# Kernel optimization log

Measured on AMD Instinct MI355X. Metric: run time of the kernel, lower is better.

The kernel has to match this reference:

```python
import jax, jax.numpy as jnp
import numpy as np

B, L, D, K = 1024, 50, 128, 20
NI, NL, NT = 100000, 10000, 2000  # items, locs, times


def _emb(k, n, d):
    e = jax.random.normal(k, (n, d), dtype=jnp.float32) * 0.02
    return e.at[0].set(0.0)  # padding_idx=0


def setup_inputs() -> dict:
    key = jax.random.key(0)
    ks = jax.random.split(key, 40)
    inp = {}
    inp['item'] = jax.random.randint(ks[0], (B, L), 0, NI)
    inp['locs'] = jax.random.randint(ks[1], (B,), 0, NL)
    inp['times'] = jax.random.randint(ks[2], (B,), 0, NT)
    inp['session_emb'] = jax.random.normal(ks[3], (B, 1, D), dtype=jnp.float32)
    # embedding tables
    inp['loc_emb'] = _emb(ks[4], NL, D)
    inp['time_emb'] = _emb(ks[5], NT, D)
    inp['item_emb'] = _emb(ks[6], NI, D)
    # sampled fixed-fanout neighbor tables Hg[edge]['neighbor']
    inp['nb_IL'] = jax.random.randint(ks[7], (NL, K), 0, NI)   # item neighbors of locs
    inp['nb_TL'] = jax.random.randint(ks[8], (NL, K), 0, NT)   # time neighbors of locs
    inp['nb_IT'] = jax.random.randint(ks[9], (NT, K), 0, NI)   # item neighbors of times
    inp['nb_LT'] = jax.random.randint(ks[10], (NT, K), 0, NL)  # loc neighbors of times
    inp['nb_II'] = jax.random.randint(ks[11], (NI, K), 0, NI)  # item neighbors of items
    inp['nb_LI'] = jax.random.randint(ks[12], (NI, K), 0, NL)  # loc neighbors of items
    inp['nb_TI'] = jax.random.randint(ks[13], (NI, K), 0, NT)  # time neighbors of items
    # 7 HeteAggregator params: Linear(2D -> D) + ReLU
    s = 1.0 / np.sqrt(2 * D)
    names = ['IL', 'TL', 'IT', 'LT', 'II', 'LI', 'TI']
    for i, nm in enumerate(names):
        inp['W_' + nm] = jax.random.uniform(ks[14 + i], (2 * D, D), jnp.float32, -s, s)
        inp['b_' + nm] = jnp.zeros((D,), jnp.float32)
    # 3 SemanticAttention params: Linear(D->D,bias)+tanh, Linear(D->1,no bias)
    s2 = 1.0 / np.sqrt(D)
    for i, nm in enumerate(['l', 't', 'i']):
        inp['Ws_' + nm] = jax.random.uniform(ks[24 + 3 * i], (D, D), jnp.float32, -s2, s2)
        inp['bs_' + nm] = jnp.zeros((D,), jnp.float32)
        inp['q_' + nm] = jax.random.uniform(ks[25 + 3 * i], (D, 1), jnp.float32, -s2, s2)
    return inp


def hete_agg(h_self, h_neigh, W, b):
    # h_self: [N, D]; h_neigh: [N, K, D] -> mean-aggregate, concat, linear, relu
    agg = h_neigh.mean(axis=1)
    return jax.nn.relu(jnp.concatenate([h_self, agg], axis=-1) @ W + b)


def sem_att(z, Ws, bs, q):
    # HAN-style semantic attention. z: [N, M, D]
    w = jnp.tanh(z @ Ws + bs) @ q          # [N, M, 1]
    beta = jax.nn.softmax(w.mean(axis=0), axis=0)  # [M, 1]
    return (beta[None] * z).sum(axis=1)    # [N, D]


def reference(item, locs, times, session_emb,
              loc_emb, time_emb, item_emb,
              nb_IL, nb_TL, nb_IT, nb_LT, nb_II, nb_LI, nb_TI,
              W_IL, b_IL, W_TL, b_TL, W_IT, b_IT, W_LT, b_LT,
              W_II, b_II, W_LI, b_LI, W_TI, b_TI,
              Ws_l, bs_l, q_l, Ws_t, bs_t, q_t, Ws_i, bs_i, q_i):
    iids = item.reshape(-1)  # [B*L]
    h_l_IL = hete_agg(loc_emb[locs], item_emb[nb_IL[locs]], W_IL, b_IL)
    h_l_TL = hete_agg(loc_emb[locs], time_emb[nb_TL[locs]], W_TL, b_TL)
    h_t_IT = hete_agg(time_emb[times], item_emb[nb_IT[times]], W_IT, b_IT)
    h_t_LT = hete_agg(time_emb[times], loc_emb[nb_LT[times]], W_LT, b_LT)
    h_i_II = hete_agg(item_emb[iids], item_emb[nb_II[iids]], W_II, b_II)
    h_i_LI = hete_agg(item_emb[iids], loc_emb[nb_LI[iids]], W_LI, b_LI)
    h_i_TI = hete_agg(item_emb[iids], time_emb[nb_TI[iids]], W_TI, b_TI)
    h_s = session_emb.squeeze(1)  # [B, D]
    h_l_stack = jnp.stack([h_l_IL, h_l_TL, h_s], axis=1)
    h_t_stack = jnp.stack([h_t_IT, h_t_LT, h_s], axis=1)
    h_i_stack = jnp.stack([h_i_II, h_i_TI, h_i_LI], axis=1)
    h_items = sem_att(h_i_stack, Ws_i, bs_i, q_i)
    h_locs = sem_att(h_l_stack, Ws_l, bs_l, q_l)
    h_times = sem_att(h_t_stack, Ws_t, bs_t, q_t)
    return (h_items, h_locs, h_times)
```

## Files before the change

### kernel.cpp

```cpp
#include <hip/hip_runtime.h>
#include <hip/hip_fp16.h>

#define DD 128
#define KK 20
#define TRR 16

typedef unsigned int uint_t;
typedef unsigned short ushort_t;
typedef unsigned char uchar_t;
typedef _Float16 f16x8 __attribute__((ext_vector_type(8)));
typedef _Float16 f16x2 __attribute__((ext_vector_type(2)));
typedef float f32x4 __attribute__((ext_vector_type(4)));
typedef float f32x2 __attribute__((ext_vector_type(2)));

union UH { __half h; ushort_t s; };
union UF { f16x2 v[4]; uint4 u4; };

#if __has_builtin(__builtin_amdgcn_cvt_scalef32_pk_f16_fp8)
#define HAVE_SCALEF32 1
#endif

__device__ __forceinline__ float fast_tanh(float x) {
  const float e = __expf(2.f * x);
  return 1.f - 2.f / (e + 1.f);
}

__device__ __forceinline__ void f8acc(f16x2* a, const uint2 v) {
#ifdef HAVE_SCALEF32
  a[0] += __builtin_amdgcn_cvt_scalef32_pk_f16_fp8(v.x, 1.0f, false);
  a[1] += __builtin_amdgcn_cvt_scalef32_pk_f16_fp8(v.x, 1.0f, true);
  a[2] += __builtin_amdgcn_cvt_scalef32_pk_f16_fp8(v.y, 1.0f, false);
  a[3] += __builtin_amdgcn_cvt_scalef32_pk_f16_fp8(v.y, 1.0f, true);
#else
  f32x2 p;
  p = __builtin_amdgcn_cvt_pk_f32_fp8(v.x, false);
  a[0] += __builtin_amdgcn_cvt_pkrtz(p[0], p[1]);
  p = __builtin_amdgcn_cvt_pk_f32_fp8(v.x, true);
  a[1] += __builtin_amdgcn_cvt_pkrtz(p[0], p[1]);
  p = __builtin_amdgcn_cvt_pk_f32_fp8(v.y, false);
  a[2] += __builtin_amdgcn_cvt_pkrtz(p[0], p[1]);
  p = __builtin_amdgcn_cvt_pk_f32_fp8(v.y, true);
  a[3] += __builtin_amdgcn_cvt_pkrtz(p[0], p[1]);
#endif
}

struct CvtArgs {
  const float* item; const float* loc; const float* timet;
  ushort_t* dst16; uchar_t* dst8;
};

__global__ __launch_bounds__(256)
void k_cvt3(CvtArgs a) {
  const int t = blockIdx.x * blockDim.x + threadIdx.x;
  const float* src;
  if (t < 1600000) src = a.item + (size_t)t * 8;
  else if (t < 1760000) src = a.loc + ((size_t)t - 1600000) * 8;
  else src = a.timet + ((size_t)t - 1760000) * 8;
  const float4* ip = reinterpret_cast<const float4*>(src);
  const float4 x = ip[0], y = ip[1];
  UH h[8];
  h[0].h = __float2half_rn(x.x); h[1].h = __float2half_rn(x.y);
  h[2].h = __float2half_rn(x.z); h[3].h = __float2half_rn(x.w);
  h[4].h = __float2half_rn(y.x); h[5].h = __float2half_rn(y.y);
  h[6].h = __float2half_rn(y.z); h[7].h = __float2half_rn(y.w);
  uint4 o;
  o.x = (uint_t)h[0].s | ((uint_t)h[1].s << 16);
  o.y = (uint_t)h[2].s | ((uint_t)h[3].s << 16);
  o.z = (uint_t)h[4].s | ((uint_t)h[5].s << 16);
  o.w = (uint_t)h[6].s | ((uint_t)h[7].s << 16);
  reinterpret_cast<uint4*>(a.dst16)[t] = o;
  uint_t p0 = __builtin_amdgcn_cvt_pk_fp8_f32(x.x, x.y, 0u, false);
  p0 = __builtin_amdgcn_cvt_pk_fp8_f32(x.z, x.w, p0, true);
  uint_t p1 = __builtin_amdgcn_cvt_pk_fp8_f32(y.x, y.y, 0u, false);
  p1 = __builtin_amdgcn_cvt_pk_fp8_f32(y.z, y.w, p1, true);
  uint2 q; q.x = p0; q.y = p1;
  reinterpret_cast<uint2*>(a.dst8)[t] = q;
}

struct PackArgs {
  const float* src[10];
  ushort_t* dst;
};

__global__ __launch_bounds__(256)
void k_pack10(PackArgs a) {
  const int b = blockIdx.x, tid = threadIdx.x;
  int job, tin;
  size_t doff;
  if (b < 112) {
    job = b >> 4; tin = ((b & 15) << 8) | tid;
    doff = (size_t)job * 32768;
  } else {
    job = 7 + ((b - 112) >> 3); tin = (((b - 112) & 7) << 8) | tid;
    doff = 7ull * 32768 + (size_t)(job - 7) * 16384;
  }
  const float* W = a.src[job];
  const int l = tin & 63;
  const int ktnt = tin >> 6;
  const int nt = ktnt & 7;
  const int kt = ktnt >> 3;
  const int col = nt * 16 + (l & 15);
  const int kb = kt * 32 + ((l >> 4) << 3);
  UH h[8];
#pragma unroll
  for (int j = 0; j < 8; ++j) h[j].h = __float2half_rn(W[(size_t)(kb + j) * DD + col]);
  uint4 o;
  o.x = (uint_t)h[0].s | ((uint_t)h[1].s << 16);
  o.y = (uint_t)h[2].s | ((uint_t)h[3].s << 16);
  o.z = (uint_t)h[4].s | ((uint_t)h[5].s << 16);
  o.w = (uint_t)h[6].s | ((uint_t)h[7].s << 16);
  *reinterpret_cast<uint4*>(a.dst + doff + (size_t)ktnt * 512 + l * 8) = o;
}

struct MegaArgs {
  const int* item_idx; const ushort_t* item_t;
  const int* nbI[3]; const uchar_t* embI[3]; const ushort_t* pWI[3]; const float* bI[3];
  const ushort_t* pWsI; const float* bsI; const float* qI;
  ushort_t* hI; float* wsumI;
  const int* sidx[2]; const ushort_t* st[2];
  const int* nbS[2][2]; const uchar_t* embS[2][2];
  const ushort_t* pWS[2][2]; const float* bS[2][2];
  const ushort_t* pWsS[2]; const float* bsS[2]; const float* qS[2];
  const float* session;
  ushort_t* hS[2]; float* wsumS[2];
};

__global__ __launch_bounds__(256, 7)
void k_mega(MegaArgs a) {
  __shared__ int ids[TRR];
  __shared__ int nidx[3][TRR][KK];
  __shared__ __align__(16) ushort_t xs[TRR][4 * DD + 8];
  __shared__ float red[4][TRR];

  const int tid = threadIdx.x;
  const int l = tid & 63;
  const int w = tid >> 6;
  const int bid = blockIdx.x;

  const bool isS = bid < 128;
  const int g = isS ? (bid >> 6) : 0;
  const int bl = isS ? (bid & 63) : (bid - 128);
  const int n0 = bl * TRR;

  const int* sidx;
  const ushort_t* selft;
  const int* nb_[3];
  const uchar_t* emb_[3];
  const ushort_t* pW_[3];
  const float* bias_[3];
  const ushort_t* pws; const float* bss; const float* qp;
  ushort_t* hd; float* wbase;
  if (!isS) {
    sidx = a.item_idx; selft = a.item_t;
    nb_[0] = a.nbI[0]; nb_[1] = a.nbI[1]; nb_[2] = a.nbI[2];
    emb_[0] = a.embI[0]; emb_[1] = a.embI[1]; emb_[2] = a.embI[2];
    pW_[0] = a.pWI[0]; pW_[1] = a.pWI[1]; pW_[2] = a.pWI[2];
    bias_[0] = a.bI[0]; bias_[1] = a.bI[1]; bias_[2] = a.bI[2];
    pws = a.pWsI; bss = a.bsI; qp = a.qI;
    hd = a.hI; wbase = a.wsumI;
  } else if (g == 0) {
    sidx = a.sidx[0]; selft = a.st[0];
    nb_[0] = a.nbS[0][0]; nb_[1] = a.nbS[0][1]; nb_[2] = nullptr;
    emb_[0] = a.embS[0][0]; emb_[1] = a.embS[0][1]; emb_[2] = nullptr;
    pW_[0] = a.pWS[0][0]; pW_[1] = a.pWS[0][1]; pW_[2] = nullptr;
    bias_[0] = a.bS[0][0]; bias_[1] = a.bS[0][1]; bias_[2] = nullptr;
    pws = a.pWsS[0]; bss = a.bsS[0]; qp = a.qS[0];
    hd = a.hS[0]; wbase = a.wsumS[0];
  } else {
    sidx = a.sidx[1]; selft = a.st[1];
    nb_[0] = a.nbS[1][0]; nb_[1] = a.nbS[1][1]; nb_[2] = nullptr;
    emb_[0] = a.embS[1][0]; emb_[1] = a.embS[1][1]; emb_[2] = nullptr;
    pW_[0] = a.pWS[1][0]; pW_[1] = a.pWS[1][1]; pW_[2] = nullptr;
    bias_[0] = a.bS[1][0]; bias_[1] = a.bS[1][1]; bias_[2] = nullptr;
    pws = a.pWsS[1]; bss = a.bsS[1]; qp = a.qS[1];
    hd = a.hS[1]; wbase = a.wsumS[1];
  }

  if (tid < TRR) ids[tid] = sidx[n0 + tid];
  __syncthreads();

  const int gr = tid >> 4;
  const int gsl = tid & 15;

#pragma unroll
  for (int e = 0; e < 3; ++e) {
    if (nb_[e]) {
      for (int t = tid; t < TRR * KK; t += 256) {
        const int rr = t / KK, kk = t - rr * KK;
        nidx[e][rr][kk] = nb_[e][(size_t)ids[rr] * KK + kk];
      }
    }
  }
  *reinterpret_cast<uint4*>(&xs[gr][gsl * 8]) =
      *reinterpret_cast<const uint4*>(selft + ((size_t)ids[gr] << 7) + gsl * 8);
  __syncthreads();

  const _Float16 sch = (_Float16)(1.f / KK);
  const f16x2 scv = (f16x2){sch, sch};
  if (!isS) {
    UF A0, A1, A2;
#pragma unroll
    for (int i = 0; i < 4; ++i) {
      A0.v[i] = (f16x2)0; A1.v[i] = (f16x2)0; A2.v[i] = (f16x2)0;
    }
#pragma unroll
    for (int kb = 0; kb < KK; kb += 4) {
      uint2 u0[4], u1[4], u2[4];
#pragma unroll
      for (int j = 0; j < 4; ++j)
        u0[j] = *reinterpret_cast<const uint2*>(emb_[0] + ((size_t)nidx[0][gr][kb + j] << 7) + gsl * 8);
#pragma unroll
      for (int j = 0; j < 4; ++j)
        u1[j] = *reinterpret_cast<const uint2*>(emb_[1] + ((size_t)nidx[1][gr][kb + j] << 7) + gsl * 8);
#pragma unroll
      for (int j = 0; j < 4; ++j)
        u2[j] = *reinterpret_cast<const uint2*>(emb_[2] + ((size_t)nidx[2][gr][kb + j] << 7) + gsl * 8);
#pragma unroll
      for (int j = 0; j < 4; ++j) {
        f8acc(A0.v, u0[j]); f8acc(A1.v, u1[j]); f8acc(A2.v, u2[j]);
      }
    }
#pragma unroll
    for (int i = 0; i < 4; ++i) {
      A0.v[i] *= scv; A1.v[i] *= scv; A2.v[i] *= scv;
    }
    *reinterpret_cast<uint4*>(&xs[gr][1 * DD + gsl * 8]) = A0.u4;
    *reinterpret_cast<uint4*>(&xs[gr][2 * DD + gsl * 8]) = A1.u4;
    *reinterpret_cast<uint4*>(&xs[gr][3 * DD + gsl * 8]) = A2.u4;
  } else {
    UF A0, A1;
#pragma unroll
    for (int i = 0; i < 4; ++i) { A0.v[i] = (f16x2)0; A1.v[i] = (f16x2)0; }
#pragma unroll
    for (int kb = 0; kb < KK; kb += 5) {
      uint2 u0[5], u1[5];
#pragma unroll
      for (int j = 0; j < 5; ++j)
        u0[j] = *reinterpret_cast<const uint2*>(emb_[0] + ((size_t)nidx[0][gr][kb + j] << 7) + gsl * 8);
#pragma unroll
      for (int j = 0; j < 5; ++j)
        u1[j] = *reinterpret_cast<const uint2*>(emb_[1] + ((size_t)nidx[1][gr][kb + j] << 7) + gsl * 8);
#pragma unroll
      for (int j = 0; j < 5; ++j) { f8acc(A0.v, u0[j]); f8acc(A1.v, u1[j]); }
    }
#pragma unroll
    for (int i = 0; i < 4; ++i) { A0.v[i] *= scv; A1.v[i] *= scv; }
    *reinterpret_cast<uint4*>(&xs[gr][1 * DD + gsl * 8]) = A0.u4;
    *reinterpret_cast<uint4*>(&xs[gr][2 * DD + gsl * 8]) = A1.u4;
    const float* srow = a.session + (size_t)(n0 + gr) * DD + gsl * 8;
    const float4 v0 = *reinterpret_cast<const float4*>(srow);
    const float4 v1 = *reinterpret_cast<const float4*>(srow + 4);
    UH h0, h1, h2, h3, h4, h5, h6, h7;
    h0.h = __float2half_rn(v0.x); h1.h = __float2half_rn(v0.y);
    h2.h = __float2half_rn(v0.z); h3.h = __float2half_rn(v0.w);
    h4.h = __float2half_rn(v1.x); h5.h = __float2half_rn(v1.y);
    h6.h = __float2half_rn(v1.z); h7.h = __float2half_rn(v1.w);
    uint4 o;
    o.x = (uint_t)h0.s | ((uint_t)h1.s << 16);
    o.y = (uint_t)h2.s | ((uint_t)h3.s << 16);
    o.z = (uint_t)h4.s | ((uint_t)h5.s << 16);
    o.w = (uint_t)h6.s | ((uint_t)h7.s << 16);
    *reinterpret_cast<uint4*>(&xs[gr][3 * DD + gsl * 8]) = o;
    *reinterpret_cast<uint4*>(hd + (size_t)(n0 + gr) * 3 * DD + 2 * DD + gsl * 8) = o;
  }
  __syncthreads();

  const int nt0 = 2 * w;
  const int lcol = l & 15;
  const int g8 = (l >> 4) << 3;
  const int col0 = nt0 * 16 + lcol;
  const int col1 = col0 + 16;

#pragma unroll
  for (int e = 0; e < 3; ++e) {
    const bool full = (!isS) || (e < 2);
    if (full) {
      const ushort_t* pWp = pW_[e];
      const float* bp = bias_[e];
      f32x4 acc0, acc1;
      {
        const float b0 = bp[col0], b1 = bp[col1];
        acc0 = (f32x4){b0, b0, b0, b0};
        acc1 = (f32x4){b1, b1, b1, b1};
#pragma unroll
        for (int kt = 0; kt < 8; ++kt) {
          const int xcol = (kt < 4) ? (kt * 32 + g8) : (e * DD + kt * 32 + g8);
          const f16x8 A = *reinterpret_cast<const f16x8*>((const void*)&xs[lcol][xcol]);
          const f16x8 B0 = *reinterpret_cast<const f16x8*>(
              (const void*)(pWp + ((size_t)(kt * 8 + nt0) * 512) + l * 8));
          const f16x8 B1 = *reinterpret_cast<const f16x8*>(
              (const void*)(pWp + ((size_t)(kt * 8 + nt0 + 1) * 512) + l * 8));
          acc0 = __builtin_amdgcn_mfma_f32_16x16x32_f16(A, B0, acc0, 0, 0, 0);
          acc1 = __builtin_amdgcn_mfma_f32_16x16x32_f16(A, B1, acc1, 0, 0, 0);
        }
#pragma unroll
        for (int j = 0; j < 4; ++j) {
          acc0[j] = fmaxf(acc0[j], 0.f);
          acc1[j] = fmaxf(acc1[j], 0.f);
        }
      }
      __syncthreads();
      {
        const int rbase = (l >> 4) << 2;
#pragma unroll
        for (int j = 0; j < 4; ++j) {
          const int row = rbase + j;
          UH h0, h1;
          h0.h = __float2half_rn(acc0[j]);
          h1.h = __float2half_rn(acc1[j]);
          hd[(size_t)(n0 + row) * 3 * DD + e * DD + col0] = h0.s;
          hd[(size_t)(n0 + row) * 3 * DD + e * DD + col1] = h1.s;
          xs[row][(e + 1) * DD + col0] = h0.s;
          xs[row][(e + 1) * DD + col1] = h1.s;
        }
      }
      __syncthreads();
    }
    {
      const float b0 = bss[col0], b1 = bss[col1];
      f32x4 s0 = (f32x4){b0, b0, b0, b0};
      f32x4 s1 = (f32x4){b1, b1, b1, b1};
#pragma unroll
      for (int kt = 0; kt < 4; ++kt) {
        const f16x8 A = *reinterpret_cast<const f16x8*>(
            (const void*)&xs[lcol][(e + 1) * DD + kt * 32 + g8]);
        const f16x8 B0 = *reinterpret_cast<const f16x8*>(
            (const void*)(pws + ((size_t)(kt * 8 + nt0) * 512) + l * 8));
        const f16x8 B1 = *reinterpret_cast<const f16x8*>(
            (const void*)(pws + ((size_t)(kt * 8 + nt0 + 1) * 512) + l * 8));
        s0 = __builtin_amdgcn_mfma_f32_16x16x32_f16(A, B0, s0, 0, 0, 0);
        s1 = __builtin_amdgcn_mfma_f32_16x16x32_f16(A, B1, s1, 0, 0, 0);
      }
      const float q0 = qp[col0], q1 = qp[col1];
      float p[4];
#pragma unroll
      for (int j = 0; j < 4; ++j)
        p[j] = fast_tanh(s0[j]) * q0 + fast_tanh(s1[j]) * q1;
#pragma unroll
      for (int off = 1; off < 16; off <<= 1) {
#pragma unroll
        for (int j = 0; j < 4; ++j) p[j] += __shfl_xor(p[j], off, 64);
      }
      if (lcol == 0) {
        const int rbase = (l >> 4) << 2;
#pragma unroll
        for (int j = 0; j < 4; ++j) red[w][rbase + j] = p[j];
      }
    }
    __syncthreads();
    if (tid < TRR) {
      float s = red[0][tid] + red[1][tid] + red[2][tid] + red[3][tid];
#pragma unroll
      for (int off = 1; off < 16; off <<= 1) s += __shfl_xor(s, off, 64);
      if (tid == 0) atomicAdd(&wbase[(bl & 63) * 4 + e], s);
    }
    __syncthreads();
  }
}

__global__ void k_beta(const float* __restrict__ wsum, float* __restrict__ beta) {
  if (threadIdx.x == 0 && blockIdx.x == 0) {
    const float invN[3] = {1.f / 51200.f, 1.f / 1024.f, 1.f / 1024.f};
    for (int g = 0; g < 3; ++g) {
      float s0 = 0.f, s1 = 0.f, s2 = 0.f;
      for (int bkt = 0; bkt < 64; ++bkt) {
        s0 += wsum[g * 256 + bkt * 4 + 0];
        s1 += wsum[g * 256 + bkt * 4 + 1];
        s2 += wsum[g * 256 + bkt * 4 + 2];
      }
      s0 *= invN[g]; s1 *= invN[g]; s2 *= invN[g];
      const float mx = fmaxf(s0, fmaxf(s1, s2));
      const float e0 = expf(s0 - mx), e1 = expf(s1 - mx), e2 = expf(s2 - mx);
      const float inv = 1.f / (e0 + e1 + e2);
      beta[g * 4 + 0] = e0 * inv;
      beta[g * 4 + 1] = e1 * inv;
      beta[g * 4 + 2] = e2 * inv;
    }
  }
}

__global__ void k_out(const ushort_t* __restrict__ h, const float* __restrict__ beta,
                      float* __restrict__ out) {
  const int idx = blockIdx.x * blockDim.x + threadIdx.x;
  const int row = idx >> 7;
  const int g = (row < 51200) ? 0 : ((row < 52224) ? 1 : 2);
  const float* bt = beta + g * 4;
  const size_t base = (size_t)idx + (size_t)row * 2 * DD;
  UH a, b, c;
  a.s = h[base]; b.s = h[base + DD]; c.s = h[base + 2 * DD];
  out[idx] = bt[0] * __half2float(a.h) + bt[1] * __half2float(b.h) +
             bt[2] * __half2float(c.h);
}


extern "C" void kernel_launch(void* const* d_in, const int* in_sizes, int n_in,
                              void* d_out, int out_size, void* d_ws, size_t ws_size,
                              hipStream_t stream) {
  const int*   item     = (const int*)  d_in[0];
  const int*   locs     = (const int*)  d_in[1];
  const int*   times    = (const int*)  d_in[2];
  const float* session  = (const float*)d_in[3];
  const float* loc_emb  = (const float*)d_in[4];
  const float* time_emb = (const float*)d_in[5];
  const float* item_emb = (const float*)d_in[6];
  const int* nb_IL = (const int*)d_in[7];
  const int* nb_TL = (const int*)d_in[8];
  const int* nb_IT = (const int*)d_in[9];
  const int* nb_LT = (const int*)d_in[10];
  const int* nb_II = (const int*)d_in[11];
  const int* nb_LI = (const int*)d_in[12];
  const int* nb_TI = (const int*)d_in[13];
  const float* W_IL = (const float*)d_in[14]; const float* b_IL = (const float*)d_in[15];
  const float* W_TL = (const float*)d_in[16]; const float* b_TL = (const float*)d_in[17];
  const float* W_IT = (const float*)d_in[18]; const float* b_IT = (const float*)d_in[19];
  const float* W_LT = (const float*)d_in[20]; const float* b_LT = (const float*)d_in[21];
  const float* W_II = (const float*)d_in[22]; const float* b_II = (const float*)d_in[23];
  const float* W_LI = (const float*)d_in[24]; const float* b_LI = (const float*)d_in[25];
  const float* W_TI = (const float*)d_in[26]; const float* b_TI = (const float*)d_in[27];
  const float* Ws_l = (const float*)d_in[28]; const float* bs_l = (const float*)d_in[29];
  const float* q_l  = (const float*)d_in[30];
  const float* Ws_t = (const float*)d_in[31]; const float* bs_t = (const float*)d_in[32];
  const float* q_t  = (const float*)d_in[33];
  const float* Ws_i = (const float*)d_in[34]; const float* bs_i = (const float*)d_in[35];
  const float* q_i  = (const float*)d_in[36];

  float* outp = (float*)d_out;

  char* wsb = (char*)d_ws;
  float* wsum  = (float*)wsb;
  float* betap = (float*)wsb + 1024;
  ushort_t* pk = (ushort_t*)(wsb + 16384);
  ushort_t* pk_II = pk;
  ushort_t* pk_TI = pk_II + 32768;
  ushort_t* pk_LI = pk_TI + 32768;
  ushort_t* pk_IL = pk_LI + 32768;
  ushort_t* pk_TL = pk_IL + 32768;
  ushort_t* pk_IT = pk_TL + 32768;
  ushort_t* pk_LT = pk_IT + 32768;
  ushort_t* pk_Wi = pk_LT + 32768;
  ushort_t* pk_Wl = pk_Wi + 16384;
  ushort_t* pk_Wt = pk_Wl + 16384;
  ushort_t* hbuf  = pk_Wt + 16384;
  ushort_t* item_h = hbuf + (size_t)53248 * 3 * DD;
  ushort_t* loc_h  = item_h + (size_t)100000 * DD;
  ushort_t* time_h = loc_h + (size_t)10000 * DD;
  uchar_t* item_8 = (uchar_t*)(time_h + (size_t)2000 * DD);
  uchar_t* loc_8  = item_8 + (size_t)100000 * DD;
  uchar_t* time_8 = loc_8 + (size_t)10000 * DD;

  hipMemsetAsync(d_ws, 0, 16384, stream);

  CvtArgs ca;
  ca.item = item_emb; ca.loc = loc_emb; ca.timet = time_emb;
  ca.dst16 = item_h; ca.dst8 = item_8;
  k_cvt3<<<dim3(7000), dim3(256), 0, stream>>>(ca);

  PackArgs pa;
  pa.src[0] = W_II; pa.src[1] = W_TI; pa.src[2] = W_LI;
  pa.src[3] = W_IL; pa.src[4] = W_TL; pa.src[5] = W_IT; pa.src[6] = W_LT;
  pa.src[7] = Ws_i; pa.src[8] = Ws_l; pa.src[9] = Ws_t;
  pa.dst = pk;
  k_pack10<<<dim3(136), dim3(256), 0, stream>>>(pa);

  ushort_t* h_items = hbuf;
  ushort_t* h_locs  = hbuf + (size_t)51200 * 3 * DD;
  ushort_t* h_times = hbuf + (size_t)52224 * 3 * DD;

  MegaArgs ma;
  ma.item_idx = item; ma.item_t = item_h;
  ma.nbI[0] = nb_II; ma.nbI[1] = nb_TI; ma.nbI[2] = nb_LI;
  ma.embI[0] = item_8; ma.embI[1] = time_8; ma.embI[2] = loc_8;
  ma.pWI[0] = pk_II; ma.pWI[1] = pk_TI; ma.pWI[2] = pk_LI;
  ma.bI[0] = b_II; ma.bI[1] = b_TI; ma.bI[2] = b_LI;
  ma.pWsI = pk_Wi; ma.bsI = bs_i; ma.qI = q_i;
  ma.hI = h_items; ma.wsumI = wsum + 0;
  ma.sidx[0] = locs;  ma.sidx[1] = times;
  ma.st[0] = loc_h;   ma.st[1] = time_h;
  ma.nbS[0][0] = nb_IL; ma.nbS[0][1] = nb_TL;
  ma.nbS[1][0] = nb_IT; ma.nbS[1][1] = nb_LT;
  ma.embS[0][0] = item_8; ma.embS[0][1] = time_8;
  ma.embS[1][0] = item_8; ma.embS[1][1] = loc_8;
  ma.pWS[0][0] = pk_IL; ma.pWS[0][1] = pk_TL;
  ma.pWS[1][0] = pk_IT; ma.pWS[1][1] = pk_LT;
  ma.bS[0][0] = b_IL; ma.bS[0][1] = b_TL;
  ma.bS[1][0] = b_IT; ma.bS[1][1] = b_LT;
  ma.pWsS[0] = pk_Wl; ma.pWsS[1] = pk_Wt;
  ma.bsS[0] = bs_l; ma.bsS[1] = bs_t;
  ma.qS[0] = q_l; ma.qS[1] = q_t;
  ma.session = session;
  ma.hS[0] = h_locs; ma.hS[1] = h_times;
  ma.wsumS[0] = wsum + 256; ma.wsumS[1] = wsum + 512;
  k_mega<<<dim3(128 + 51200 / TRR), dim3(256), 0, stream>>>(ma);

  k_beta<<<dim3(1), dim3(64), 0, stream>>>(wsum, betap);
  k_out<<<dim3((53248 * 128) / 256), dim3(256), 0, stream>>>(hbuf, betap, outp);
}
```

Measured before the change: 123.6 us.

## Double rows per block and share weight fragments across two MFMA row tiles

Raises rows per block from 16 to 32 and threads from 256 to 512, so there are 8 waves. Each wave now owns a single 16-column output tile and issues MFMAs for two 16-row tiles against the same B fragment. This is meant to halve weight-fragment loads per row in both the aggregator and semantic-attention GEMMs, and to halve the number of blocks and atomics. In exchange, blocks are larger and use more LDS, the launch bounds drop to 6 blocks per unit, and the attention reduction is widened to 32 rows.

```diff
diff --git a/kernel.cpp b/kernel.cpp
--- a/kernel.cpp
+++ b/kernel.cpp
@@ -3,7 +3,8 @@
 
 #define DD 128
 #define KK 20
-#define TRR 16
+#define TRR 32
+#define NT 512
 
 typedef unsigned int uint_t;
 typedef unsigned short ushort_t;
@@ -125,21 +126,21 @@
   ushort_t* hS[2]; float* wsumS[2];
 };
 
-__global__ __launch_bounds__(256, 7)
+__global__ __launch_bounds__(NT, 6)
 void k_mega(MegaArgs a) {
   __shared__ int ids[TRR];
   __shared__ int nidx[3][TRR][KK];
   __shared__ __align__(16) ushort_t xs[TRR][4 * DD + 8];
-  __shared__ float red[4][TRR];
+  __shared__ float red[8][TRR];
 
   const int tid = threadIdx.x;
   const int l = tid & 63;
   const int w = tid >> 6;
   const int bid = blockIdx.x;
 
-  const bool isS = bid < 128;
-  const int g = isS ? (bid >> 6) : 0;
-  const int bl = isS ? (bid & 63) : (bid - 128);
+  const bool isS = bid < 64;
+  const int g = isS ? (bid >> 5) : 0;
+  const int bl = isS ? (bid & 31) : (bid - 64);
   const int n0 = bl * TRR;
 
   const int* sidx;
@@ -185,7 +186,7 @@
 #pragma unroll
   for (int e = 0; e < 3; ++e) {
     if (nb_[e]) {
-      for (int t = tid; t < TRR * KK; t += 256) {
+      for (int t = tid; t < TRR * KK; t += NT) {
         const int rr = t / KK, kk = t - rr * KK;
         nidx[e][rr][kk] = nb_[e][(size_t)ids[rr] * KK + kk];
       }
@@ -265,11 +266,9 @@
   }
   __syncthreads();
 
-  const int nt0 = 2 * w;
   const int lcol = l & 15;
   const int g8 = (l >> 4) << 3;
-  const int col0 = nt0 * 16 + lcol;
-  const int col1 = col0 + 16;
+  const int col0 = w * 16 + lcol;
 
 #pragma unroll
   for (int e = 0; e < 3; ++e) {
@@ -279,19 +278,18 @@
       const float* bp = bias_[e];
       f32x4 acc0, acc1;
       {
-        const float b0 = bp[col0], b1 = bp[col1];
+        const float b0 = bp[col0];
         acc0 = (f32x4){b0, b0, b0, b0};
-        acc1 = (f32x4){b1, b1, b1, b1};
+        acc1 = acc0;
 #pragma unroll
         for (int kt = 0; kt < 8; ++kt) {
           const int xcol = (kt < 4) ? (kt * 32 + g8) : (e * DD + kt * 32 + g8);
-          const f16x8 A = *reinterpret_cast<const f16x8*>((const void*)&xs[lcol][xcol]);
-          const f16x8 B0 = *reinterpret_cast<const f16x8*>(
-              (const void*)(pWp + ((size_t)(kt * 8 + nt0) * 512) + l * 8));
-          const f16x8 B1 = *reinterpret_cast<const f16x8*>(
-              (const void*)(pWp + ((size_t)(kt * 8 + nt0 + 1) * 512) + l * 8));
-          acc0 = __builtin_amdgcn_mfma_f32_16x16x32_f16(A, B0, acc0, 0, 0, 0);
-          acc1 = __builtin_amdgcn_mfma_f32_16x16x32_f16(A, B1, acc1, 0, 0, 0);
+          const f16x8 Aa = *reinterpret_cast<const f16x8*>((const void*)&xs[lcol][xcol]);
+          const f16x8 Ab = *reinterpret_cast<const f16x8*>((const void*)&xs[16 + lcol][xcol]);
+          const f16x8 B = *reinterpret_cast<const f16x8*>(
+              (const void*)(pWp + ((size_t)(kt * 8 + w) * 512) + l * 8));
+          acc0 = __builtin_amdgcn_mfma_f32_16x16x32_f16(Aa, B, acc0, 0, 0, 0);
+          acc1 = __builtin_amdgcn_mfma_f32_16x16x32_f16(Ab, B, acc1, 0, 0, 0);
         }
 #pragma unroll
         for (int j = 0; j < 4; ++j) {
@@ -304,54 +302,64 @@
         const int rbase = (l >> 4) << 2;
 #pragma unroll
         for (int j = 0; j < 4; ++j) {
-          const int row = rbase + j;
+          const int r0 = rbase + j, r1 = 16 + rbase + j;
           UH h0, h1;
           h0.h = __float2half_rn(acc0[j]);
           h1.h = __float2half_rn(acc1[j]);
-          hd[(size_t)(n0 + row) * 3 * DD + e * DD + col0] = h0.s;
-          hd[(size_t)(n0 + row) * 3 * DD + e * DD + col1] = h1.s;
-          xs[row][(e + 1) * DD + col0] = h0.s;
-          xs[row][(e + 1) * DD + col1] = h1.s;
+          hd[(size_t)(n0 + r0) * 3 * DD + e * DD + col0] = h0.s;
+          hd[(size_t)(n0 + r1) * 3 * DD + e * DD + col0] = h1.s;
+          xs[r0][(e + 1) * DD + col0] = h0.s;
+          xs[r1][(e + 1) * DD + col0] = h1.s;
         }
       }
       __syncthreads();
     }
     {
-      const float b0 = bss[col0], b1 = bss[col1];
+      const float b0 = bss[col0];
       f32x4 s0 = (f32x4){b0, b0, b0, b0};
-      f32x4 s1 = (f32x4){b1, b1, b1, b1};
+      f32x4 s1 = s0;
 #pragma unroll
       for (int kt = 0; kt < 4; ++kt) {
-        const f16x8 A = *reinterpret_cast<const f16x8*>(
+        const f16x8 Aa = *reinterpret_cast<const f16x8*>(
             (const void*)&xs[lcol][(e + 1) * DD + kt * 32 + g8]);
-        const f16x8 B0 = *reinterpret_cast<const f16x8*>(
-            (const void*)(pws + ((size_t)(kt * 8 + nt0) * 512) + l * 8));
-        const f16x8 B1 = *reinterpret_cast<const f16x8*>(
-            (const void*)(pws + ((size_t)(kt * 8 + nt0 + 1) * 512) + l * 8));
-        s0 = __builtin_amdgcn_mfma_f32_16x16x32_f16(A, B0, s0, 0, 0, 0);
-        s1 = __builtin_amdgcn_mfma_f32_16x16x32_f16(A, B1, s1, 0, 0, 0);
-      }
-      const float q0 = qp[col0], q1 = qp[col1];
-      float p[4];
-#pragma unroll
-      for (int j = 0; j < 4; ++j)
-        p[j] = fast_tanh(s0[j]) * q0 + fast_tanh(s1[j]) * q1;
+        const f16x8 Ab = *reinterpret_cast<const f16x8*>(
+            (const void*)&xs[16 + lcol][(e + 1) * DD + kt * 32 + g8]);
+        const f16x8 B = *reinterpret_cast<const f16x8*>(
+            (const void*)(pws + ((size_t)(kt * 8 + w) * 512) + l * 8));
+        s0 = __builtin_amdgcn_mfma_f32_16x16x32_f16(Aa, B, s0, 0, 0, 0);
+        s1 = __builtin_amdgcn_mfma_f32_16x16x32_f16(Ab, B, s1, 0, 0, 0);
+      }
+      const float q0 = qp[col0];
+      float p0[4], p1[4];
+#pragma unroll
+      for (int j = 0; j < 4; ++j) {
+        p0[j] = fast_tanh(s0[j]) * q0;
+        p1[j] = fast_tanh(s1[j]) * q0;
+      }
 #pragma unroll
       for (int off = 1; off < 16; off <<= 1) {
 #pragma unroll
-        for (int j = 0; j < 4; ++j) p[j] += __shfl_xor(p[j], off, 64);
+        for (int j = 0; j < 4; ++j) {
+          p0[j] += __shfl_xor(p0[j], off, 64);
+          p1[j] += __shfl_xor(p1[j], off, 64);
+        }
       }
       if (lcol == 0) {
         const int rbase = (l >> 4) << 2;
 #pragma unroll
-        for (int j = 0; j < 4; ++j) red[w][rbase + j] = p[j];
+        for (int j = 0; j < 4; ++j) {
+          red[w][rbase + j] = p0[j];
+          red[w][16 + rbase + j] = p1[j];
+        }
       }
     }
     __syncthreads();
     if (tid < TRR) {
-      float s = red[0][tid] + red[1][tid] + red[2][tid] + red[3][tid];
-#pragma unroll
-      for (int off = 1; off < 16; off <<= 1) s += __shfl_xor(s, off, 64);
+      float s = 0.f;
+#pragma unroll
+      for (int ww = 0; ww < 8; ++ww) s += red[ww][tid];
+#pragma unroll
+      for (int off = 1; off < 32; off <<= 1) s += __shfl_xor(s, off, 64);
       if (tid == 0) atomicAdd(&wbase[(bl & 63) * 4 + e], s);
     }
     __syncthreads();
@@ -490,7 +498,7 @@
   ma.session = session;
   ma.hS[0] = h_locs; ma.hS[1] = h_times;
   ma.wsumS[0] = wsum + 256; ma.wsumS[1] = wsum + 512;
-  k_mega<<<dim3(128 + 51200 / TRR), dim3(256), 0, stream>>>(ma);
+  k_mega<<<dim3(64 + 51200 / TRR), dim3(NT), 0, stream>>>(ma);
 
   k_beta<<<dim3(1), dim3(64), 0, stream>>>(wsum, betap);
   k_out<<<dim3((53248 * 128) / 256), dim3(256), 0, stream>>>(hbuf, betap, outp);
```

Measured after the change: 123.0 us. About the same (-0.4%).
